# Performance work log

Hardware: AMD Instinct MI355X
Metric: run time of the kernel (lower is better)

The kernel has to match this reference:

```python
import jax, jax.numpy as jnp
import numpy as np

LN_EPS = 1e-5

def _layernorm(x, w, b):
    mu = jnp.mean(x, axis=-1, keepdims=True)
    var = jnp.mean(jnp.square(x - mu), axis=-1, keepdims=True)
    return (x - mu) * jax.lax.rsqrt(var + LN_EPS) * w + b

def setup_inputs() -> dict:
    key = jax.random.key(0)
    ks = jax.random.split(key, 6)
    B, NQ, QD = 8, 576, 4096
    NKV, KVD = 2304, 1024
    s = 0.02
    return {
        "x_q": jax.random.normal(ks[0], (B, NQ, QD), jnp.float32),
        "x_kv": jax.random.normal(ks[1], (B, NKV, KVD), jnp.float32),
        "q_ln_w": jnp.ones((QD,), jnp.float32),
        "q_ln_b": jnp.zeros((QD,), jnp.float32),
        "q_w": jax.random.normal(ks[2], (QD, QD), jnp.float32) * s,
        "q_b": jnp.zeros((QD,), jnp.float32),
        "k_ln_w": jnp.ones((KVD,), jnp.float32),
        "k_ln_b": jnp.zeros((KVD,), jnp.float32),
        "k_w": jax.random.normal(ks[3], (KVD, QD), jnp.float32) * s,
        "k_b": jnp.zeros((QD,), jnp.float32),
        "v_ln_w": jnp.ones((KVD,), jnp.float32),
        "v_ln_b": jnp.zeros((KVD,), jnp.float32),
        "v_w": jax.random.normal(ks[4], (KVD, QD), jnp.float32) * s,
        "v_b": jnp.zeros((QD,), jnp.float32),
    }

def reference(x_q, x_kv, q_ln_w, q_ln_b, q_w, q_b,
              k_ln_w, k_ln_b, k_w, k_b, v_ln_w, v_ln_b, v_w, v_b):
    B, NQ, QD = x_q.shape
    hw = int(round(x_kv.shape[1] ** 0.5))          # 48
    KVD = x_kv.shape[-1]
    patch_num = int(round(NQ ** 0.5))              # 24
    patch_size = hw // patch_num                   # 2
    # 'b (h w) d -> b h w d' then group into patch_num x patch_num windows
    kv = x_kv.reshape(B, hw, hw, KVD)
    kv = kv.reshape(B, patch_num, patch_size, patch_num, patch_size, KVD)
    kv = kv.transpose(0, 1, 3, 2, 4, 5).reshape(B, patch_num * patch_num, patch_size * patch_size, KVD)
    # projections (LayerNorm + Linear)
    q = _layernorm(x_q, q_ln_w, q_ln_b) @ q_w + q_b            # [B, P2, QD]
    k = _layernorm(kv, k_ln_w, k_ln_b) @ k_w + k_b             # [B, P2, S2, QD]
    v = _layernorm(kv, v_ln_w, v_ln_b) @ v_w + v_b             # [B, P2, S2, QD]
    scale = 1.0 / (QD ** 0.5)
    att = jnp.einsum('bpd,bpsd->bps', q, k) * scale            # [B, P2, S2]
    att = jnp.nan_to_num(att)
    att = jax.nn.softmax(att, axis=-1)
    feat = jnp.einsum('bps,bpsd->bpd', att, v)                 # [B, P2, QD]
    return (x_q, feat)
```

## Files before the change

### kernel.cpp

```cpp
#include <hip/hip_runtime.h>
#include <cstdint>
#include <cstddef>


typedef __attribute__((ext_vector_type(8))) short short8;
typedef __attribute__((ext_vector_type(4))) float f32x4;

#define DEV __device__ __forceinline__

DEV unsigned short f2bf(float f) {
  union { float f; unsigned u; } x; x.f = f;
  unsigned r = x.u + 0x7fffu + ((x.u >> 16) & 1u);
  return (unsigned short)(r >> 16);
}
DEV float bf2f(unsigned short u) {
  union { unsigned u; float f; } x; x.u = ((unsigned)u) << 16;
  return x.f;
}

DEV void gload16(const void* g, void* l) {
  __builtin_amdgcn_global_load_lds(
      (const __attribute__((address_space(1))) unsigned int*)g,
      (__attribute__((address_space(3))) unsigned int*)l, 16, 0, 0);
}

template <bool PARTIAL, bool HAS_BIAS>
__global__ __launch_bounds__(256, 2) void gemm_nt(
    const unsigned short* __restrict__ A, const unsigned short* __restrict__ Bm,
    void* __restrict__ Cv, const float* __restrict__ bias, int M, int N,
    int Kfull, int Kchunk) {
  __shared__ __align__(16) unsigned short lds_a[128 * 64];
  __shared__ __align__(16) unsigned short lds_b[128 * 64];
  const int t = threadIdx.x;
  const int l = t & 63;
  const int w = t >> 6;

  int bx = blockIdx.x, by = blockIdx.y;
  {
    const int nbx = gridDim.x, nby = gridDim.y;
    const int nwg = nbx * nby;
    int flat = by * nbx + bx;
    flat = (flat & 7) * (nwg >> 3) + (flat >> 3);
    bx = flat % nbx;
    by = flat / nbx;
  }
  const long brow = (long)bx * 128;
  const long bcol = (long)by * 128;
  const int z = blockIdx.z;
  const int k0 = z * Kchunk;

  const int srow0 = t >> 3;
  const int gsrc = (t & 7) ^ ((t >> 3) & 7);
  const unsigned short* aS[4];
  const unsigned short* bS[4];
  unsigned short* aD[4];
  unsigned short* bD[4];
#pragma unroll
  for (int j = 0; j < 4; ++j) {
    const long row = srow0 + 32 * j;
    aS[j] = A + (brow + row) * (long)Kfull + k0 + gsrc * 8;
    bS[j] = Bm + (bcol + row) * (long)Kfull + k0 + gsrc * 8;
    aD[j] = lds_a + (t + 256 * j) * 8;
    bD[j] = lds_b + (t + 256 * j) * 8;
  }

  const int wr = w >> 1, wc = w & 1;
  const int fr = l & 15;
  const int xr = fr & 7;
  const int gq0 = l >> 4;

  f32x4 acc[4][4] = {};

  for (int kt = 0; kt < Kchunk; kt += 64) {
    __syncthreads();
#pragma unroll
    for (int j = 0; j < 4; ++j) {
      gload16(aS[j] + kt, aD[j]);
      gload16(bS[j] + kt, bD[j]);
    }
    asm volatile("s_waitcnt vmcnt(0)" ::: "memory");
    __syncthreads();
#pragma unroll
    for (int ks = 0; ks < 2; ++ks) {
      const int gx = ((ks * 4 + gq0) ^ xr) * 8;
      short8 af[4], bfr[4];
#pragma unroll
      for (int mi = 0; mi < 4; ++mi)
        af[mi] = *(const short8*)&lds_a[(wr * 64 + mi * 16 + fr) * 64 + gx];
#pragma unroll
      for (int ni = 0; ni < 4; ++ni)
        bfr[ni] = *(const short8*)&lds_b[(wc * 64 + ni * 16 + fr) * 64 + gx];
#pragma unroll
      for (int mi = 0; mi < 4; ++mi)
#pragma unroll
        for (int ni = 0; ni < 4; ++ni)
          acc[mi][ni] = __builtin_amdgcn_mfma_f32_16x16x32_bf16(
              af[mi], bfr[ni], acc[mi][ni], 0, 0, 0);
    }
  }

  const int crow = (l >> 4) * 4;
  unsigned short* Cpart =
      PARTIAL ? ((unsigned short*)Cv + (size_t)z * M * (size_t)N) : nullptr;
#pragma unroll
  for (int ni = 0; ni < 4; ++ni) {
    const long col = bcol + wc * 64 + ni * 16 + fr;
    const float bv = (!PARTIAL && HAS_BIAS) ? bias[col] : 0.0f;
#pragma unroll
    for (int mi = 0; mi < 4; ++mi) {
#pragma unroll
      for (int r = 0; r < 4; ++r) {
        const long row = brow + wr * 64 + mi * 16 + crow + r;
        const float v = acc[mi][ni][r] + bv;
        if (PARTIAL)
          Cpart[row * (long)N + col] = f2bf(v);
        else
          ((float*)Cv)[row * (long)N + col] = v;
      }
    }
  }
}

__global__ __launch_bounds__(256) void reduce_splits_bf16(
    const unsigned short* __restrict__ part, unsigned short* __restrict__ out,
    int S, size_t MN) {
  size_t i = (size_t)blockIdx.x * 256 + threadIdx.x;
  const size_t n4 = MN / 4;
  const size_t stride = (size_t)gridDim.x * 256;
  for (; i < n4; i += stride) {
    float a0 = 0.f, a1 = 0.f, a2 = 0.f, a3 = 0.f;
    for (int s = 0; s < S; ++s) {
      const ushort4 b = ((const ushort4*)(part + (size_t)s * MN))[i];
      a0 += bf2f(b.x); a1 += bf2f(b.y); a2 += bf2f(b.z); a3 += bf2f(b.w);
    }
    ((ushort4*)out)[i] = make_ushort4(f2bf(a0), f2bf(a1), f2bf(a2), f2bf(a3));
  }
}

__global__ __launch_bounds__(256) void ln_q_kernel(
    const float* __restrict__ x, const float* __restrict__ w,
    const float* __restrict__ b, float* __restrict__ copy_out,
    unsigned short* __restrict__ qn) {
  const int row = blockIdx.x, t = threadIdx.x;
  const float4* xr = (const float4*)(x + (size_t)row * 4096);
  float4 v[4];
  float s = 0.f, s2 = 0.f;
#pragma unroll
  for (int j = 0; j < 4; ++j) {
    v[j] = xr[j * 256 + t];
    s += v[j].x + v[j].y + v[j].z + v[j].w;
    s2 += v[j].x * v[j].x + v[j].y * v[j].y + v[j].z * v[j].z + v[j].w * v[j].w;
  }
#pragma unroll
  for (int off = 32; off; off >>= 1) {
    s += __shfl_xor(s, off);
    s2 += __shfl_xor(s2, off);
  }
  __shared__ float red[8];
  if ((t & 63) == 0) { red[t >> 6] = s; red[4 + (t >> 6)] = s2; }
  __syncthreads();
  s = red[0] + red[1] + red[2] + red[3];
  s2 = red[4] + red[5] + red[6] + red[7];
  const float mu = s * (1.f / 4096.f);
  const float rstd = rsqrtf(s2 * (1.f / 4096.f) - mu * mu + 1e-5f);
  float4* co = (float4*)(copy_out + (size_t)row * 4096);
  unsigned short* qr = qn + (size_t)row * 4096;
#pragma unroll
  for (int j = 0; j < 4; ++j) {
    co[j * 256 + t] = v[j];
    const int c = (j * 256 + t) * 4;
    const float4 wv = *(const float4*)(w + c);
    const float4 bv = *(const float4*)(b + c);
    ushort4 o = make_ushort4(f2bf((v[j].x - mu) * rstd * wv.x + bv.x),
                             f2bf((v[j].y - mu) * rstd * wv.y + bv.y),
                             f2bf((v[j].z - mu) * rstd * wv.z + bv.z),
                             f2bf((v[j].w - mu) * rstd * wv.w + bv.w));
    *(ushort4*)(qr + c) = o;
  }
}

__global__ __launch_bounds__(256) void ln_kv_kernel(
    const float* __restrict__ x, const float* __restrict__ kw,
    const float* __restrict__ kb, const float* __restrict__ vw,
    const float* __restrict__ vb, unsigned short* __restrict__ kn,
    unsigned short* __restrict__ vn) {
  const int row = blockIdx.x, t = threadIdx.x;
  const float4 v = ((const float4*)(x + (size_t)row * 1024))[t];
  float s = v.x + v.y + v.z + v.w;
  float s2 = v.x * v.x + v.y * v.y + v.z * v.z + v.w * v.w;
#pragma unroll
  for (int off = 32; off; off >>= 1) {
    s += __shfl_xor(s, off);
    s2 += __shfl_xor(s2, off);
  }
  __shared__ float red[8];
  if ((t & 63) == 0) { red[t >> 6] = s; red[4 + (t >> 6)] = s2; }
  __syncthreads();
  s = red[0] + red[1] + red[2] + red[3];
  s2 = red[4] + red[5] + red[6] + red[7];
  const float mu = s * (1.f / 1024.f);
  const float rstd = rsqrtf(s2 * (1.f / 1024.f) - mu * mu + 1e-5f);
  const int c = t * 4;
  const float4 kw4 = *(const float4*)(kw + c);
  const float4 kb4 = *(const float4*)(kb + c);
  const float4 vw4 = *(const float4*)(vw + c);
  const float4 vb4 = *(const float4*)(vb + c);
  const float h0 = (v.x - mu) * rstd, h1 = (v.y - mu) * rstd;
  const float h2 = (v.z - mu) * rstd, h3 = (v.w - mu) * rstd;
  *(ushort4*)(kn + (size_t)row * 1024 + c) =
      make_ushort4(f2bf(h0 * kw4.x + kb4.x), f2bf(h1 * kw4.y + kb4.y),
                   f2bf(h2 * kw4.z + kb4.z), f2bf(h3 * kw4.w + kb4.w));
  *(ushort4*)(vn + (size_t)row * 1024 + c) =
      make_ushort4(f2bf(h0 * vw4.x + vb4.x), f2bf(h1 * vw4.y + vb4.y),
                   f2bf(h2 * vw4.z + vb4.z), f2bf(h3 * vw4.w + vb4.w));
}

__global__ __launch_bounds__(256) void conv_bf16(
    const float* __restrict__ src, unsigned short* __restrict__ dst, int n4) {
  int i = blockIdx.x * 256 + threadIdx.x;
  const int stride = gridDim.x * 256;
  for (; i < n4; i += stride) {
    const float4 v = ((const float4*)src)[i];
    ((ushort4*)dst)[i] = make_ushort4(f2bf(v.x), f2bf(v.y), f2bf(v.z), f2bf(v.w));
  }
}

__global__ __launch_bounds__(256) void conv_kw_qkb(
    const float* __restrict__ kw, const float* __restrict__ qb,
    unsigned short* __restrict__ kwb, float* __restrict__ qkb) {
  const int c = blockIdx.x, t = threadIdx.x;
  const float4* kr = (const float4*)(kw + (size_t)c * 4096);
  const float4* q4 = (const float4*)qb;
  ushort4* ko = (ushort4*)(kwb + (size_t)c * 4096);
  float s = 0.f;
#pragma unroll
  for (int j = 0; j < 4; ++j) {
    const float4 a = q4[j * 256 + t], b = kr[j * 256 + t];
    ko[j * 256 + t] = make_ushort4(f2bf(b.x), f2bf(b.y), f2bf(b.z), f2bf(b.w));
    s += a.x * b.x + a.y * b.y + a.z * b.z + a.w * b.w;
  }
#pragma unroll
  for (int off = 32; off; off >>= 1) s += __shfl_xor(s, off);
  __shared__ float red[4];
  if ((t & 63) == 0) red[t >> 6] = s;
  __syncthreads();
  if (t == 0) qkb[c] = red[0] + red[1] + red[2] + red[3];
}

__global__ void transpose_conv(const float* __restrict__ src,
                               unsigned short* __restrict__ dst) {
  __shared__ float tile[32][33];
  const int n0 = blockIdx.x * 32, k0 = blockIdx.y * 32;
  const int tx = threadIdx.x, ty = threadIdx.y;
#pragma unroll
  for (int i = 0; i < 32; i += 8)
    tile[ty + i][tx] = src[(size_t)(k0 + ty + i) * 4096 + n0 + tx];
  __syncthreads();
#pragma unroll
  for (int i = 0; i < 32; i += 8)
    dst[(size_t)(n0 + ty + i) * 1024 + k0 + tx] = f2bf(tile[tx][ty + i]);
}

__global__ __launch_bounds__(256) void att_fused(
    const unsigned short* __restrict__ part, int S, size_t PMN,
    const float* __restrict__ qkb, const unsigned short* __restrict__ kn,
    const unsigned short* __restrict__ vn, unsigned short* __restrict__ wkv) {
  const int m = blockIdx.x;
  const int b = m / 576, p = m % 576;
  const int py = p / 24, px = p % 24;
  const int t = threadIdx.x, w = t >> 6, l = t & 63;
  const int c = t * 4;
  const size_t off = (size_t)m * 1024 + c;

  const float4 qb4 = *(const float4*)(qkb + c);
  float4 q = qb4;
  for (int s = 0; s < S; ++s) {
    const ushort4 pp = *(const ushort4*)(part + (size_t)s * PMN + off);
    q.x += bf2f(pp.x); q.y += bf2f(pp.y); q.z += bf2f(pp.z); q.w += bf2f(pp.w);
  }

  size_t rows[4];
#pragma unroll
  for (int s = 0; s < 4; ++s)
    rows[s] = ((size_t)b * 2304 + (size_t)(py * 2 + (s >> 1)) * 48 +
               (px * 2 + (s & 1))) * 1024;

  float dot[4];
#pragma unroll
  for (int s = 0; s < 4; ++s) {
    const ushort4 k4 = *(const ushort4*)(kn + rows[s] + c);
    dot[s] = q.x * bf2f(k4.x) + q.y * bf2f(k4.y) + q.z * bf2f(k4.z) +
             q.w * bf2f(k4.w);
  }
#pragma unroll
  for (int s = 0; s < 4; ++s)
#pragma unroll
    for (int o = 32; o; o >>= 1) dot[s] += __shfl_xor(dot[s], o);

  __shared__ float red[4][4];
  if (l == 0) {
#pragma unroll
    for (int s = 0; s < 4; ++s) red[w][s] = dot[s];
  }
  __syncthreads();
  float lg[4];
#pragma unroll
  for (int s = 0; s < 4; ++s)
    lg[s] = (red[0][s] + red[1][s] + red[2][s] + red[3][s]) * 0.015625f;
  const float mx = fmaxf(fmaxf(lg[0], lg[1]), fmaxf(lg[2], lg[3]));
  float e[4];
#pragma unroll
  for (int s = 0; s < 4; ++s) e[s] = __expf(lg[s] - mx);
  const float inv = 1.f / (e[0] + e[1] + e[2] + e[3]);

  float a0 = 0.f, a1 = 0.f, a2 = 0.f, a3 = 0.f;
#pragma unroll
  for (int s = 0; s < 4; ++s) {
    const float at = e[s] * inv;
    const ushort4 v4 = *(const ushort4*)(vn + rows[s] + c);
    a0 += at * bf2f(v4.x);
    a1 += at * bf2f(v4.y);
    a2 += at * bf2f(v4.z);
    a3 += at * bf2f(v4.w);
  }
  *(ushort4*)(wkv + off) =
      make_ushort4(f2bf(a0), f2bf(a1), f2bf(a2), f2bf(a3));
}

extern "C" void kernel_launch(void* const* d_in, const int* in_sizes, int n_in,
                              void* d_out, int out_size, void* d_ws,
                              size_t ws_size, hipStream_t stream) {
  const float* x_q = (const float*)d_in[0];
  const float* x_kv = (const float*)d_in[1];
  const float* q_ln_w = (const float*)d_in[2];
  const float* q_ln_b = (const float*)d_in[3];
  const float* q_w = (const float*)d_in[4];
  const float* q_b = (const float*)d_in[5];
  const float* k_ln_w = (const float*)d_in[6];
  const float* k_ln_b = (const float*)d_in[7];
  const float* k_w = (const float*)d_in[8];
  const float* v_ln_w = (const float*)d_in[10];
  const float* v_ln_b = (const float*)d_in[11];
  const float* v_w = (const float*)d_in[12];
  const float* v_b = (const float*)d_in[13];

  char* ws = (char*)d_ws;
  unsigned short* qn = (unsigned short*)(ws);
  unsigned short* kn = (unsigned short*)(ws + 37748736);
  unsigned short* vn = (unsigned short*)(ws + 75497472);
  unsigned short* qwb = (unsigned short*)(ws + 113246208);
  unsigned short* kwb = (unsigned short*)(ws + 146800640);
  unsigned short* Wt = (unsigned short*)(ws + 155189248);
  unsigned short* vwT = (unsigned short*)(ws + 163577856);
  float* qkbv = (float*)(ws + 190840832);
  unsigned short* wkv = (unsigned short*)(ws + 190844928);
  unsigned short* part = (unsigned short*)(ws + 200282112);

  const size_t MN_W = (size_t)1024 * 4096;
  const size_t MN_QK = (size_t)4608 * 1024;
  int splitW = 1, splitQK = 1;
  if (ws_size >= 200282112ull + 4 * MN_QK * 2) { splitW = 2; splitQK = 4; }
  else if (ws_size >= 200282112ull + 2 * MN_QK * 2) { splitW = 2; splitQK = 2; }

  float* out0 = (float*)d_out;
  float* out1 = out0 + (size_t)4608 * 4096;

  ln_q_kernel<<<4608, 256, 0, stream>>>(x_q, q_ln_w, q_ln_b, out0, qn);
  ln_kv_kernel<<<18432, 256, 0, stream>>>(x_kv, k_ln_w, k_ln_b, v_ln_w, v_ln_b,
                                          kn, vn);
  conv_bf16<<<4096, 256, 0, stream>>>(q_w, qwb, 4096 * 4096 / 4);
  conv_kw_qkb<<<1024, 256, 0, stream>>>(k_w, q_b, kwb, qkbv);
  transpose_conv<<<dim3(128, 32), dim3(32, 8), 0, stream>>>(v_w, vwT);

  gemm_nt<true, false><<<dim3(8, 32, splitW), 256, 0, stream>>>(
      kwb, qwb, part, nullptr, 1024, 4096, 4096, 4096 / splitW);
  reduce_splits_bf16<<<2048, 256, 0, stream>>>(part, Wt, splitW, MN_W);

  gemm_nt<true, false><<<dim3(36, 8, splitQK), 256, 0, stream>>>(
      qn, Wt, part, nullptr, 4608, 1024, 4096, 4096 / splitQK);
  att_fused<<<4608, 256, 0, stream>>>(part, splitQK, MN_QK, qkbv, kn, vn, wkv);

  gemm_nt<false, true><<<dim3(36, 32), 256, 0, stream>>>(
      wkv, vwT, out1, v_b, 4608, 4096, 1024, 1024);
}
```

Baseline: 551.4 us.

## Use 256x256 double-buffered GEMM tiles and fold LayerNorm affine into weights

```diff
diff --git a/kernel.cpp b/kernel.cpp
--- a/kernel.cpp
+++ b/kernel.cpp
@@ -25,15 +25,15 @@
 }
 
 template <bool PARTIAL, bool HAS_BIAS>
-__global__ __launch_bounds__(256, 2) void gemm_nt(
+__global__ __launch_bounds__(512, 2) void gemm_nt(
     const unsigned short* __restrict__ A, const unsigned short* __restrict__ Bm,
     void* __restrict__ Cv, const float* __restrict__ bias, int M, int N,
     int Kfull, int Kchunk) {
-  __shared__ __align__(16) unsigned short lds_a[128 * 64];
-  __shared__ __align__(16) unsigned short lds_b[128 * 64];
+  __shared__ __align__(16) unsigned short lds_a[2][256 * 64];
+  __shared__ __align__(16) unsigned short lds_b[2][256 * 64];
   const int t = threadIdx.x;
   const int l = t & 63;
-  const int w = t >> 6;
+  const int wid = t >> 6;
 
   int bx = blockIdx.x, by = blockIdx.y;
   {
@@ -44,8 +44,8 @@
     bx = flat % nbx;
     by = flat / nbx;
   }
-  const long brow = (long)bx * 128;
-  const long bcol = (long)by * 128;
+  const long brow = (long)bx * 256;
+  const long bcol = (long)by * 256;
   const int z = blockIdx.z;
   const int k0 = z * Kchunk;
 
@@ -53,50 +53,60 @@
   const int gsrc = (t & 7) ^ ((t >> 3) & 7);
   const unsigned short* aS[4];
   const unsigned short* bS[4];
-  unsigned short* aD[4];
-  unsigned short* bD[4];
 #pragma unroll
   for (int j = 0; j < 4; ++j) {
-    const long row = srow0 + 32 * j;
+    const long row = srow0 + 64 * j;
     aS[j] = A + (brow + row) * (long)Kfull + k0 + gsrc * 8;
     bS[j] = Bm + (bcol + row) * (long)Kfull + k0 + gsrc * 8;
-    aD[j] = lds_a + (t + 256 * j) * 8;
-    bD[j] = lds_b + (t + 256 * j) * 8;
-  }
-
-  const int wr = w >> 1, wc = w & 1;
+  }
+  const int dOff = t * 8;
+
+  const int wr = wid >> 2, wc = wid & 3;
   const int fr = l & 15;
   const int xr = fr & 7;
   const int gq0 = l >> 4;
 
-  f32x4 acc[4][4] = {};
-
+  f32x4 acc[8][4] = {};
+
+#pragma unroll
+  for (int j = 0; j < 4; ++j) {
+    gload16(aS[j], &lds_a[0][dOff + 4096 * j]);
+    gload16(bS[j], &lds_b[0][dOff + 4096 * j]);
+  }
+  asm volatile("s_waitcnt vmcnt(0)" ::: "memory");
+  __syncthreads();
+
+  int cur = 0;
   for (int kt = 0; kt < Kchunk; kt += 64) {
-    __syncthreads();
-#pragma unroll
-    for (int j = 0; j < 4; ++j) {
-      gload16(aS[j] + kt, aD[j]);
-      gload16(bS[j] + kt, bD[j]);
+    const int nxt = cur ^ 1;
+    if (kt + 64 < Kchunk) {
+#pragma unroll
+      for (int j = 0; j < 4; ++j) {
+        gload16(aS[j] + kt + 64, &lds_a[nxt][dOff + 4096 * j]);
+        gload16(bS[j] + kt + 64, &lds_b[nxt][dOff + 4096 * j]);
+      }
+    }
+#pragma unroll
+    for (int ks = 0; ks < 2; ++ks) {
+      const int gx = ((ks * 4 + gq0) ^ xr) * 8;
+      short8 bfr[4];
+#pragma unroll
+      for (int ni = 0; ni < 4; ++ni)
+        bfr[ni] =
+            *(const short8*)&lds_b[cur][(wc * 64 + ni * 16 + fr) * 64 + gx];
+#pragma unroll
+      for (int mi = 0; mi < 8; ++mi) {
+        const short8 af =
+            *(const short8*)&lds_a[cur][(wr * 128 + mi * 16 + fr) * 64 + gx];
+#pragma unroll
+        for (int ni = 0; ni < 4; ++ni)
+          acc[mi][ni] = __builtin_amdgcn_mfma_f32_16x16x32_bf16(
+              af, bfr[ni], acc[mi][ni], 0, 0, 0);
+      }
     }
     asm volatile("s_waitcnt vmcnt(0)" ::: "memory");
     __syncthreads();
-#pragma unroll
-    for (int ks = 0; ks < 2; ++ks) {
-      const int gx = ((ks * 4 + gq0) ^ xr) * 8;
-      short8 af[4], bfr[4];
-#pragma unroll
-      for (int mi = 0; mi < 4; ++mi)
-        af[mi] = *(const short8*)&lds_a[(wr * 64 + mi * 16 + fr) * 64 + gx];
-#pragma unroll
-      for (int ni = 0; ni < 4; ++ni)
-        bfr[ni] = *(const short8*)&lds_b[(wc * 64 + ni * 16 + fr) * 64 + gx];
-#pragma unroll
-      for (int mi = 0; mi < 4; ++mi)
-#pragma unroll
-        for (int ni = 0; ni < 4; ++ni)
-          acc[mi][ni] = __builtin_amdgcn_mfma_f32_16x16x32_bf16(
-              af[mi], bfr[ni], acc[mi][ni], 0, 0, 0);
-    }
+    cur = nxt;
   }
 
   const int crow = (l >> 4) * 4;
@@ -107,10 +117,10 @@
     const long col = bcol + wc * 64 + ni * 16 + fr;
     const float bv = (!PARTIAL && HAS_BIAS) ? bias[col] : 0.0f;
 #pragma unroll
-    for (int mi = 0; mi < 4; ++mi) {
+    for (int mi = 0; mi < 8; ++mi) {
 #pragma unroll
       for (int r = 0; r < 4; ++r) {
-        const long row = brow + wr * 64 + mi * 16 + crow + r;
+        const long row = brow + wr * 128 + mi * 16 + crow + r;
         const float v = acc[mi][ni][r] + bv;
         if (PARTIAL)
           Cpart[row * (long)N + col] = f2bf(v);
@@ -180,10 +190,7 @@
 }
 
 __global__ __launch_bounds__(256) void ln_kv_kernel(
-    const float* __restrict__ x, const float* __restrict__ kw,
-    const float* __restrict__ kb, const float* __restrict__ vw,
-    const float* __restrict__ vb, unsigned short* __restrict__ kn,
-    unsigned short* __restrict__ vn) {
+    const float* __restrict__ x, unsigned short* __restrict__ h) {
   const int row = blockIdx.x, t = threadIdx.x;
   const float4 v = ((const float4*)(x + (size_t)row * 1024))[t];
   float s = v.x + v.y + v.z + v.w;
@@ -200,19 +207,9 @@
   s2 = red[4] + red[5] + red[6] + red[7];
   const float mu = s * (1.f / 1024.f);
   const float rstd = rsqrtf(s2 * (1.f / 1024.f) - mu * mu + 1e-5f);
-  const int c = t * 4;
-  const float4 kw4 = *(const float4*)(kw + c);
-  const float4 kb4 = *(const float4*)(kb + c);
-  const float4 vw4 = *(const float4*)(vw + c);
-  const float4 vb4 = *(const float4*)(vb + c);
-  const float h0 = (v.x - mu) * rstd, h1 = (v.y - mu) * rstd;
-  const float h2 = (v.z - mu) * rstd, h3 = (v.w - mu) * rstd;
-  *(ushort4*)(kn + (size_t)row * 1024 + c) =
-      make_ushort4(f2bf(h0 * kw4.x + kb4.x), f2bf(h1 * kw4.y + kb4.y),
-                   f2bf(h2 * kw4.z + kb4.z), f2bf(h3 * kw4.w + kb4.w));
-  *(ushort4*)(vn + (size_t)row * 1024 + c) =
-      make_ushort4(f2bf(h0 * vw4.x + vb4.x), f2bf(h1 * vw4.y + vb4.y),
-                   f2bf(h2 * vw4.z + vb4.z), f2bf(h3 * vw4.w + vb4.w));
+  *(ushort4*)(h + (size_t)row * 1024 + t * 4) =
+      make_ushort4(f2bf((v.x - mu) * rstd), f2bf((v.y - mu) * rstd),
+                   f2bf((v.z - mu) * rstd), f2bf((v.w - mu) * rstd));
 }
 
 __global__ __launch_bounds__(256) void conv_bf16(
@@ -248,6 +245,7 @@
 }
 
 __global__ void transpose_conv(const float* __restrict__ src,
+                               const float* __restrict__ vlnw,
                                unsigned short* __restrict__ dst) {
   __shared__ float tile[32][33];
   const int n0 = blockIdx.x * 32, k0 = blockIdx.y * 32;
@@ -256,15 +254,33 @@
   for (int i = 0; i < 32; i += 8)
     tile[ty + i][tx] = src[(size_t)(k0 + ty + i) * 4096 + n0 + tx];
   __syncthreads();
+  const float vw_ = vlnw[k0 + tx];
 #pragma unroll
   for (int i = 0; i < 32; i += 8)
-    dst[(size_t)(n0 + ty + i) * 1024 + k0 + tx] = f2bf(tile[tx][ty + i]);
+    dst[(size_t)(n0 + ty + i) * 1024 + k0 + tx] = f2bf(tile[tx][ty + i] * vw_);
+}
+
+__global__ __launch_bounds__(256) void vb_fold(const float* __restrict__ vw_,
+                                               const float* __restrict__ vlnb,
+                                               const float* __restrict__ vb,
+                                               float* __restrict__ bias2) {
+  const int nl = threadIdx.x & 63;
+  const int seg = threadIdx.x >> 6;
+  const int n = blockIdx.x * 64 + nl;
+  float s = 0.f;
+  for (int d = seg * 256; d < seg * 256 + 256; ++d)
+    s += vlnb[d] * vw_[(size_t)d * 4096 + n];
+  __shared__ float red[4][64];
+  red[seg][nl] = s;
+  __syncthreads();
+  if (seg == 0)
+    bias2[n] = vb[n] + red[0][nl] + red[1][nl] + red[2][nl] + red[3][nl];
 }
 
 __global__ __launch_bounds__(256) void att_fused(
     const unsigned short* __restrict__ part, int S, size_t PMN,
-    const float* __restrict__ qkb, const unsigned short* __restrict__ kn,
-    const unsigned short* __restrict__ vn, unsigned short* __restrict__ wkv) {
+    const float* __restrict__ qkb, const float* __restrict__ klnw,
+    const unsigned short* __restrict__ h, unsigned short* __restrict__ mix) {
   const int m = blockIdx.x;
   const int b = m / 576, p = m % 576;
   const int py = p / 24, px = p % 24;
@@ -272,12 +288,13 @@
   const int c = t * 4;
   const size_t off = (size_t)m * 1024 + c;
 
-  const float4 qb4 = *(const float4*)(qkb + c);
-  float4 q = qb4;
+  float4 q = *(const float4*)(qkb + c);
   for (int s = 0; s < S; ++s) {
     const ushort4 pp = *(const ushort4*)(part + (size_t)s * PMN + off);
     q.x += bf2f(pp.x); q.y += bf2f(pp.y); q.z += bf2f(pp.z); q.w += bf2f(pp.w);
   }
+  const float4 kw4 = *(const float4*)(klnw + c);
+  q.x *= kw4.x; q.y *= kw4.y; q.z *= kw4.z; q.w *= kw4.w;
 
   size_t rows[4];
 #pragma unroll
@@ -285,12 +302,14 @@
     rows[s] = ((size_t)b * 2304 + (size_t)(py * 2 + (s >> 1)) * 48 +
                (px * 2 + (s & 1))) * 1024;
 
+  float hv[4][4];
   float dot[4];
 #pragma unroll
   for (int s = 0; s < 4; ++s) {
-    const ushort4 k4 = *(const ushort4*)(kn + rows[s] + c);
-    dot[s] = q.x * bf2f(k4.x) + q.y * bf2f(k4.y) + q.z * bf2f(k4.z) +
-             q.w * bf2f(k4.w);
+    const ushort4 h4 = *(const ushort4*)(h + rows[s] + c);
+    hv[s][0] = bf2f(h4.x); hv[s][1] = bf2f(h4.y);
+    hv[s][2] = bf2f(h4.z); hv[s][3] = bf2f(h4.w);
+    dot[s] = q.x * hv[s][0] + q.y * hv[s][1] + q.z * hv[s][2] + q.w * hv[s][3];
   }
 #pragma unroll
   for (int s = 0; s < 4; ++s)
@@ -317,13 +336,12 @@
 #pragma unroll
   for (int s = 0; s < 4; ++s) {
     const float at = e[s] * inv;
-    const ushort4 v4 = *(const ushort4*)(vn + rows[s] + c);
-    a0 += at * bf2f(v4.x);
-    a1 += at * bf2f(v4.y);
-    a2 += at * bf2f(v4.z);
-    a3 += at * bf2f(v4.w);
-  }
-  *(ushort4*)(wkv + off) =
+    a0 += at * hv[s][0];
+    a1 += at * hv[s][1];
+    a2 += at * hv[s][2];
+    a3 += at * hv[s][3];
+  }
+  *(ushort4*)(mix + off) =
       make_ushort4(f2bf(a0), f2bf(a1), f2bf(a2), f2bf(a3));
 }
 
@@ -337,7 +355,6 @@
   const float* q_w = (const float*)d_in[4];
   const float* q_b = (const float*)d_in[5];
   const float* k_ln_w = (const float*)d_in[6];
-  const float* k_ln_b = (const float*)d_in[7];
   const float* k_w = (const float*)d_in[8];
   const float* v_ln_w = (const float*)d_in[10];
   const float* v_ln_b = (const float*)d_in[11];
@@ -346,40 +363,41 @@
 
   char* ws = (char*)d_ws;
   unsigned short* qn = (unsigned short*)(ws);
-  unsigned short* kn = (unsigned short*)(ws + 37748736);
-  unsigned short* vn = (unsigned short*)(ws + 75497472);
+  unsigned short* h = (unsigned short*)(ws + 37748736);
+  float* bias2 = (float*)(ws + 75497472);
   unsigned short* qwb = (unsigned short*)(ws + 113246208);
   unsigned short* kwb = (unsigned short*)(ws + 146800640);
   unsigned short* Wt = (unsigned short*)(ws + 155189248);
   unsigned short* vwT = (unsigned short*)(ws + 163577856);
   float* qkbv = (float*)(ws + 190840832);
-  unsigned short* wkv = (unsigned short*)(ws + 190844928);
+  unsigned short* mix = (unsigned short*)(ws + 190844928);
   unsigned short* part = (unsigned short*)(ws + 200282112);
 
   const size_t MN_W = (size_t)1024 * 4096;
   const size_t MN_QK = (size_t)4608 * 1024;
   int splitW = 1, splitQK = 1;
-  if (ws_size >= 200282112ull + 4 * MN_QK * 2) { splitW = 2; splitQK = 4; }
+  if (ws_size >= 200282112ull + 4 * MN_QK * 2) { splitW = 4; splitQK = 4; }
   else if (ws_size >= 200282112ull + 2 * MN_QK * 2) { splitW = 2; splitQK = 2; }
 
   float* out0 = (float*)d_out;
   float* out1 = out0 + (size_t)4608 * 4096;
 
   ln_q_kernel<<<4608, 256, 0, stream>>>(x_q, q_ln_w, q_ln_b, out0, qn);
-  ln_kv_kernel<<<18432, 256, 0, stream>>>(x_kv, k_ln_w, k_ln_b, v_ln_w, v_ln_b,
-                                          kn, vn);
+  ln_kv_kernel<<<18432, 256, 0, stream>>>(x_kv, h);
   conv_bf16<<<4096, 256, 0, stream>>>(q_w, qwb, 4096 * 4096 / 4);
   conv_kw_qkb<<<1024, 256, 0, stream>>>(k_w, q_b, kwb, qkbv);
-  transpose_conv<<<dim3(128, 32), dim3(32, 8), 0, stream>>>(v_w, vwT);
-
-  gemm_nt<true, false><<<dim3(8, 32, splitW), 256, 0, stream>>>(
+  transpose_conv<<<dim3(128, 32), dim3(32, 8), 0, stream>>>(v_w, v_ln_w, vwT);
+  vb_fold<<<64, 256, 0, stream>>>(v_w, v_ln_b, v_b, bias2);
+
+  gemm_nt<true, false><<<dim3(4, 16, splitW), 512, 0, stream>>>(
       kwb, qwb, part, nullptr, 1024, 4096, 4096, 4096 / splitW);
   reduce_splits_bf16<<<2048, 256, 0, stream>>>(part, Wt, splitW, MN_W);
 
-  gemm_nt<true, false><<<dim3(36, 8, splitQK), 256, 0, stream>>>(
+  gemm_nt<true, false><<<dim3(18, 4, splitQK), 512, 0, stream>>>(
       qn, Wt, part, nullptr, 4608, 1024, 4096, 4096 / splitQK);
-  att_fused<<<4608, 256, 0, stream>>>(part, splitQK, MN_QK, qkbv, kn, vn, wkv);
-
-  gemm_nt<false, true><<<dim3(36, 32), 256, 0, stream>>>(
-      wkv, vwT, out1, v_b, 4608, 4096, 1024, 1024);
-}
+  att_fused<<<4608, 256, 0, stream>>>(part, splitQK, MN_QK, qkbv, k_ln_w, h,
+                                      mix);
+
+  gemm_nt<false, true><<<dim3(18, 16, 1), 512, 0, stream>>>(
+      mix, vwT, out1, bias2, 4608, 4096, 1024, 1024);
+}
```

New measurement: 599.5 us. 1.09x slower.
